# Kernel optimization log

Measured on AMD Instinct MI355X. Metric: run time of the kernel, lower is better.

## Reference

```python
import jax, jax.numpy as jnp
import numpy as np

B, T, C = 4, 4096, 1024
H, G = 16, 8
HS = C // H      # head size = 64
GT = T // G      # group_t = 512
KAPX = 1         # k_apx


def causal_attn(q, k, v):
    # q,k,v: [..., L, d]; causal softmax attention within last two dims
    d = q.shape[-1]
    s = jnp.einsum('...qd,...kd->...qk', q, k) / jnp.sqrt(jnp.asarray(d, q.dtype))
    mask = jnp.tril(jnp.ones((s.shape[-2], s.shape[-1]), dtype=bool))
    s = jnp.where(mask, s, jnp.asarray(-1e30, s.dtype))
    return jnp.einsum('...qk,...kd->...qd', jax.nn.softmax(s, axis=-1), v)


def apply_rope(x, cos, sin):
    # x: [B,H,T,HS]; cos/sin: [T,HS//2]; interleaved (even,odd) complex pairs
    xr = x.reshape(x.shape[:-1] + (HS // 2, 2))
    r, i = xr[..., 0], xr[..., 1]
    c = cos[None, None]
    s = sin[None, None]
    return jnp.stack([r * c - i * s, r * s + i * c], axis=-1).reshape(x.shape)


def setup_inputs() -> dict:
    key = jax.random.key(0)
    k1, k2, k3, k4, k5, k6 = jax.random.split(key, 6)
    x = jax.random.normal(k1, (B, T, C), jnp.float32)
    lim = 1.0 / np.sqrt(C)
    Wqkv = jax.random.uniform(k2, (C, 3 * C), jnp.float32, -lim, lim)
    Wo = jax.random.uniform(k3, (C, C), jnp.float32, -lim, lim)
    # init_() uses std = 1/sqrt(last_dim) = 1/sqrt(k_apx) = 1
    q_proj = jax.random.uniform(k4, (GT, KAPX), jnp.float32, -1.0, 1.0)
    k_proj = jax.random.uniform(k5, (GT, KAPX), jnp.float32, -1.0, 1.0)
    v_proj = jax.random.uniform(k6, (GT, KAPX), jnp.float32, -1.0, 1.0)
    inv = 1.0 / (10000.0 ** (np.arange(0, HS, 2) / HS))
    ang = np.outer(np.arange(T), inv)
    freqs_cos = jnp.asarray(np.cos(ang), jnp.float32)
    freqs_sin = jnp.asarray(np.sin(ang), jnp.float32)
    return dict(x=x, Wqkv=Wqkv, Wo=Wo, q_proj=q_proj, k_proj=k_proj,
                v_proj=v_proj, freqs_cos=freqs_cos, freqs_sin=freqs_sin)


def reference(x, Wqkv, Wo, q_proj, k_proj, v_proj, freqs_cos, freqs_sin):
    q, k, v = jnp.split(x @ Wqkv, 3, axis=-1)          # each [B,T,C]
    q = q.reshape(B, T, H, HS).transpose(0, 2, 1, 3)    # [B,H,T,HS]
    k = k.reshape(B, T, H, HS).transpose(0, 2, 1, 3)
    q = apply_rope(q, freqs_cos, freqs_sin)
    k = apply_rope(k, freqs_cos, freqs_sin)
    # torch .view on contiguous [B,H,T,HS]: raw row-major reinterpretation
    q = q.reshape(B, G, GT, H, HS).transpose(0, 3, 1, 2, 4)  # [B,H,G,GT,HS]
    k = k.reshape(B, G, GT, H, HS).transpose(0, 3, 1, 2, 4)
    v = v.reshape(B, G, GT, H, HS).transpose(0, 3, 1, 2, 4)  # v viewed from [B,T,C]
    # its_time branch: learned time-pooling of all but last group
    qb = jnp.einsum('bhgtc,tk->bhgkc', q[:, :, :-1], q_proj)  # [B,H,G-1,1,HS]
    kb = jnp.einsum('bhgtc,tk->bhgkc', k[:, :, :-1], k_proj)
    vb = jnp.einsum('bhgtc,tk->bhgkc', v[:, :, :-1], v_proj)
    o = causal_attn(q, k, v)          # block-local causal attention [B,H,G,GT,HS]
    vb = causal_attn(qb, kb, vb)      # compressed block attention [B,H,G-1,1,HS]
    o = o.reshape(B, H, G * GT, HS).transpose(0, 2, 1, 3).reshape(B, T, C)
    out = o @ Wo                       # dropout=0 (eval)
    return (out, qb, kb, vb)
```

## Files before the change

### kernel.cpp

```cpp
#include <hip/hip_runtime.h>


typedef float  float4_t  __attribute__((ext_vector_type(4)));
typedef short  bfrag     __attribute__((ext_vector_type(8)));
typedef unsigned short ushort8 __attribute__((ext_vector_type(8)));

#define MFMA_BF16(A, B, C) __builtin_amdgcn_mfma_f32_16x16x32_bf16((A), (B), (C), 0, 0, 0)

__device__ __forceinline__ unsigned short f2bf(float f) {
  union { float f; unsigned u; } v; v.f = f;
  return (unsigned short)((v.u + 0x7FFFu + ((v.u >> 16) & 1u)) >> 16);
}
__device__ __forceinline__ float bf2f(unsigned short h) {
  union { unsigned u; float f; } v; v.u = ((unsigned)h) << 16; return v.f;
}
__device__ __forceinline__ void async16(const void* g, void* l) {
  __builtin_amdgcn_global_load_lds(
      (const __attribute__((address_space(1))) unsigned int*)(unsigned long long)g,
      (__attribute__((address_space(3))) unsigned int*)(unsigned long long)l,
      16, 0, 0);
}

__global__ __launch_bounds__(256) void cvt_kernel(const float* __restrict__ in,
                                                  unsigned short* __restrict__ out, int n8) {
  int i = blockIdx.x * 256 + threadIdx.x;
  if (i >= n8) return;
  const float4_t* p = (const float4_t*)in + (size_t)i * 2;
  float4_t a = p[0], c = p[1];
  ushort8 r;
  r[0] = f2bf(a[0]); r[1] = f2bf(a[1]); r[2] = f2bf(a[2]); r[3] = f2bf(a[3]);
  r[4] = f2bf(c[0]); r[5] = f2bf(c[1]); r[6] = f2bf(c[2]); r[7] = f2bf(c[3]);
  *((ushort8*)out + i) = r;
}

__global__ void transpose_cvt_kernel(const float* __restrict__ in,
                                     unsigned short* __restrict__ out, int R, int C) {
  __shared__ float t[32][33];
  int bc = blockIdx.x * 32, br = blockIdx.y * 32;
  int x = threadIdx.x, y = threadIdx.y;
  for (int i = 0; i < 32; i += 8) t[y + i][x] = in[(size_t)(br + y + i) * C + bc + x];
  __syncthreads();
  for (int i = 0; i < 32; i += 8) out[(size_t)(bc + y + i) * R + br + x] = f2bf(t[x][y + i]);
}

__global__ void transpose2_f32_kernel(const float* __restrict__ a,
                                      const float* __restrict__ b,
                                      float* __restrict__ oa, float* __restrict__ ob_,
                                      int R, int C) {
  const float* in = blockIdx.z ? b : a;
  float* out = blockIdx.z ? ob_ : oa;
  __shared__ float t[32][33];
  int bc = blockIdx.x * 32, br = blockIdx.y * 32;
  int x = threadIdx.x, y = threadIdx.y;
  for (int i = 0; i < 32; i += 8) t[y + i][x] = in[(size_t)(br + y + i) * C + bc + x];
  __syncthreads();
  for (int i = 0; i < 32; i += 8) out[(size_t)(bc + y + i) * R + br + x] = t[x][y + i];
}

__device__ __forceinline__ void gemm_core(const unsigned short* __restrict__ A,
                                          const unsigned short* __restrict__ BT,
                                          int bm0, int bn0, int K,
                                          unsigned short* As, unsigned short* Bs,
                                          float4_t acc[4][4]) {
  int tid = threadIdx.x, w = tid >> 6;
  int lane = tid & 63, quad = lane >> 4, l16 = lane & 15;
  int wm = w >> 1, wn = w & 1;
  int rr = tid >> 2, xx = tid & 3;
  for (int k0 = 0; k0 < K; k0 += 32) {
    __syncthreads();
    {
      int r0 = rr,       s0 = xx ^ ((r0 >> 1) & 3);
      int r1 = rr + 64,  s1 = xx ^ ((r1 >> 1) & 3);
      async16(&A [(size_t)(bm0 + r0) * K + k0 + s0 * 8], &As[(size_t)(w * 64) * 8]);
      async16(&A [(size_t)(bm0 + r1) * K + k0 + s1 * 8], &As[(size_t)(256 + w * 64) * 8]);
      async16(&BT[(size_t)(bn0 + r0) * K + k0 + s0 * 8], &Bs[(size_t)(w * 64) * 8]);
      async16(&BT[(size_t)(bn0 + r1) * K + k0 + s1 * 8], &Bs[(size_t)(256 + w * 64) * 8]);
    }
    __syncthreads();
    bfrag af[4], bf_[4];
    for (int i = 0; i < 4; ++i) {
      int rm = wm * 64 + i * 16 + l16;
      af[i]  = *(const bfrag*)&As[(size_t)(rm * 4 + (quad ^ ((rm >> 1) & 3))) * 8];
      int rn = wn * 64 + i * 16 + l16;
      bf_[i] = *(const bfrag*)&Bs[(size_t)(rn * 4 + (quad ^ ((rn >> 1) & 3))) * 8];
    }
    for (int i = 0; i < 4; ++i)
      for (int j = 0; j < 4; ++j)
        acc[i][j] = MFMA_BF16(af[i], bf_[j], acc[i][j]);
  }
}

__global__ __launch_bounds__(256) void gemm1_kernel(const unsigned short* __restrict__ xb,
    const unsigned short* __restrict__ wqkvT,
    const float* __restrict__ fcT, const float* __restrict__ fsT,
    unsigned short* __restrict__ q5, unsigned short* __restrict__ k5,
    unsigned short* __restrict__ v5) {
  __shared__ __align__(16) unsigned short As[128 * 32];
  __shared__ __align__(16) unsigned short Bs[128 * 32];
  __shared__ __align__(16) float Es[4 * 1088];
  float4_t acc[4][4];
  for (int i = 0; i < 4; ++i) for (int j = 0; j < 4; ++j)
    acc[i][j] = (float4_t){0.f, 0.f, 0.f, 0.f};
  int bn0 = blockIdx.x * 128, bm0 = blockIdx.y * 128;
  gemm_core(xb, wqkvT, bm0, bn0, 1024, As, Bs, acc);

  int tid = threadIdx.x, w = tid >> 6, lane = tid & 63, quad = lane >> 4, l16 = lane & 15;
  int wm = w >> 1, wn = w & 1;

  for (int i = 0; i < 4; ++i) {
    int t0 = (bm0 + wm * 64 + i * 16 + quad * 4) & 4095;
    for (int j = 0; j < 4; ++j) {
      int gcol = bn0 + wn * 64 + j * 16 + l16;
      if (gcol < 2048) {
        int ci = (gcol & 63) >> 1;
        const float4_t c4 = *(const float4_t*)&fcT[(size_t)ci * 4096 + t0];
        const float4_t s4 = *(const float4_t*)&fsT[(size_t)ci * 4096 + t0];
        for (int r = 0; r < 4; ++r) {
          float val = acc[i][j][r];
          float partner = __shfl_xor(val, 1);
          float c = c4[r], s = s4[r];
          acc[i][j][r] = (gcol & 1) ? fmaf(partner, s, val * c)
                                    : fmaf(-partner, s, val * c);
        }
      }
    }
  }

  float* slice = &Es[w * 1088];
  for (int i = 0; i < 4; ++i) {
    for (int j = 0; j < 4; ++j)
      for (int r = 0; r < 4; ++r)
        slice[(quad * 4 + r) * 68 + j * 16 + l16] = acc[i][j][r];
    for (int m = 0; m < 2; ++m) {
      int rl = m * 8 + (lane >> 3);
      int cb = (lane & 7) * 8;
      const float* rp = &slice[rl * 68 + cb];
      ushort8 outv;
      outv[0] = f2bf(rp[0]); outv[1] = f2bf(rp[1]);
      outv[2] = f2bf(rp[2]); outv[3] = f2bf(rp[3]);
      outv[4] = f2bf(rp[4]); outv[5] = f2bf(rp[5]);
      outv[6] = f2bf(rp[6]); outv[7] = f2bf(rp[7]);
      int grow = bm0 + wm * 64 + i * 16 + rl;
      int b = grow >> 12, t = grow & 4095;
      int gcol = bn0 + wn * 64 + cb;
      if (gcol < 2048) {
        int cc = gcol & 1023;
        int ho = cc >> 6, hs0 = cc & 63;
        size_t idx = ((((size_t)b * 16 + (t & 15)) * 8 + (ho >> 1)) * 512 +
                      (((ho & 1) << 8) | (t >> 4))) * 64 + hs0;
        if (gcol < 1024) *(ushort8*)&q5[idx] = outv;
        else             *(ushort8*)&k5[idx] = outv;
      } else {
        int cc = gcol - 2048;
        size_t idx = ((((size_t)b * 16 + (cc >> 6)) * 8 + (t >> 9)) * 512 +
                      (t & 511)) * 64 + (cc & 63);
        *(ushort8*)&v5[idx] = outv;
      }
    }
  }
}

__global__ __launch_bounds__(256) void gemm2_kernel(const unsigned short* __restrict__ ob,
    const unsigned short* __restrict__ woT, float* __restrict__ outp) {
  __shared__ __align__(16) unsigned short As[128 * 32];
  __shared__ __align__(16) unsigned short Bs[128 * 32];
  float4_t acc[4][4];
  for (int i = 0; i < 4; ++i) for (int j = 0; j < 4; ++j)
    acc[i][j] = (float4_t){0.f, 0.f, 0.f, 0.f};
  int bn0 = blockIdx.x * 128, bm0 = blockIdx.y * 128;
  gemm_core(ob, woT, bm0, bn0, 1024, As, Bs, acc);
  int tid = threadIdx.x, w = tid >> 6, lane = tid & 63, quad = lane >> 4, l16 = lane & 15;
  int wm = w >> 1, wn = w & 1;
  for (int i = 0; i < 4; ++i)
    for (int j = 0; j < 4; ++j)
      for (int r = 0; r < 4; ++r)
        outp[(size_t)(bm0 + wm * 64 + i * 16 + quad * 4 + r) * 1024 +
             bn0 + wn * 64 + j * 16 + l16] = acc[i][j][r];
}

__global__ __launch_bounds__(256) void attn_kernel(const unsigned short* __restrict__ q5,
    const unsigned short* __restrict__ k5, const unsigned short* __restrict__ v5,
    unsigned short* __restrict__ ob) {
  __shared__ __align__(16) unsigned short Ks[128 * 64];
  __shared__ __align__(16) unsigned short VTs[64 * 136];
  __shared__ __align__(16) unsigned short Ps[4 * 16 * 136];
  int bx = blockIdx.x;
  int qt = bx & 7, g = (bx >> 3) & 7, h = (bx >> 6) & 15, b = bx >> 10;
  int tid = threadIdx.x, w = tid >> 6, lane = tid & 63, quad = lane >> 4, l16 = lane & 15;
  size_t base = ((((size_t)b * 16 + h) * 8 + g) * 512) * 64;
  const unsigned short* Q = q5 + base;
  const unsigned short* K = k5 + base;
  const unsigned short* V = v5 + base;

  int qrow = qt * 64 + w * 16 + l16;
  bfrag qf0 = *(const bfrag*)&Q[(size_t)qrow * 64 + quad * 8];
  bfrag qf1 = *(const bfrag*)&Q[(size_t)qrow * 64 + 32 + quad * 8];

  float4_t acc[4];
#pragma unroll
  for (int i = 0; i < 4; ++i) acc[i] = (float4_t){0.f, 0.f, 0.f, 0.f};
  float m_i[4] = {-1e30f, -1e30f, -1e30f, -1e30f};
  float l_i[4] = {0.f, 0.f, 0.f, 0.f};

  int skey = tid >> 3, sx = tid & 7, ss = sx ^ (skey & 7);
  int kp = tid & 63, hsg = tid >> 6;
  unsigned short* Pw = &Ps[w * 2176];
  int ntiles = (qt + 2) >> 1;

  for (int kt = 0; kt < ntiles; ++kt) {
    __syncthreads();
#pragma unroll
    for (int c = 0; c < 4; ++c)
      async16(&K[(size_t)(kt * 128 + 32 * c + skey) * 64 + ss * 8],
              &Ks[(size_t)(c * 256 + w * 64) * 8]);
    {
      const unsigned short* vp0 = &V[(size_t)(kt * 128 + kp * 2) * 64 + hsg * 16];
      ushort8 va0 = *(const ushort8*)vp0;
      ushort8 va1 = *(const ushort8*)(vp0 + 8);
      ushort8 vb0 = *(const ushort8*)(vp0 + 64);
      ushort8 vb1 = *(const ushort8*)(vp0 + 72);
#pragma unroll
      for (int e = 0; e < 8; ++e) {
        *(unsigned*)&VTs[(size_t)(hsg * 16 + e) * 136 + kp * 2] =
            (unsigned)va0[e] | ((unsigned)vb0[e] << 16);
        *(unsigned*)&VTs[(size_t)(hsg * 16 + 8 + e) * 136 + kp * 2] =
            (unsigned)va1[e] | ((unsigned)vb1[e] << 16);
      }
    }
    __syncthreads();

    float4_t s[8];
#pragma unroll
    for (int c = 0; c < 8; ++c) s[c] = (float4_t){0.f, 0.f, 0.f, 0.f};
    {
      int sl0 = l16 * 8 + (quad ^ (l16 & 7));
      int sl1 = l16 * 8 + ((4 + quad) ^ (l16 & 7));
#pragma unroll
      for (int c = 0; c < 8; ++c) {
        s[c] = MFMA_BF16(qf0, *(const bfrag*)&Ks[(size_t)(sl0 + 128 * c) * 8], s[c]);
        s[c] = MFMA_BF16(qf1, *(const bfrag*)&Ks[(size_t)(sl1 + 128 * c) * 8], s[c]);
      }
    }

    int qa = qt * 64 + w * 16 + quad * 4;
    int kb0 = kt * 128 + l16;
#pragma unroll
    for (int r = 0; r < 4; ++r) {
      float vv[8];
#pragma unroll
      for (int c = 0; c < 8; ++c) {
        vv[c] = s[c][r] * 0.125f;
        if (kb0 + 16 * c > qa + r) vv[c] = -1e30f;
      }
      float tm = fmaxf(fmaxf(fmaxf(vv[0], vv[1]), fmaxf(vv[2], vv[3])),
                       fmaxf(fmaxf(vv[4], vv[5]), fmaxf(vv[6], vv[7])));
      tm = fmaxf(tm, __shfl_xor(tm, 1));
      tm = fmaxf(tm, __shfl_xor(tm, 2));
      tm = fmaxf(tm, __shfl_xor(tm, 4));
      tm = fmaxf(tm, __shfl_xor(tm, 8));
      float nm = fmaxf(m_i[r], tm);
      float alpha = __expf(m_i[r] - nm);
      m_i[r] = nm;
      float p[8], rs = 0.f;
#pragma unroll
      for (int c = 0; c < 8; ++c) { p[c] = __expf(vv[c] - nm); rs += p[c]; }
      rs += __shfl_xor(rs, 1);
      rs += __shfl_xor(rs, 2);
      rs += __shfl_xor(rs, 4);
      rs += __shfl_xor(rs, 8);
      l_i[r] = l_i[r] * alpha + rs;
      acc[0][r] *= alpha; acc[1][r] *= alpha; acc[2][r] *= alpha; acc[3][r] *= alpha;
      int pr = (quad * 4 + r) * 136 + l16;
#pragma unroll
      for (int c = 0; c < 8; ++c) Pw[pr + 16 * c] = f2bf(p[c]);
    }
    bfrag pf[4];
#pragma unroll
    for (int c = 0; c < 4; ++c)
      pf[c] = *(const bfrag*)&Pw[(size_t)l16 * 136 + 32 * c + quad * 8];
#pragma unroll
    for (int ht = 0; ht < 4; ++ht) {
#pragma unroll
      for (int c = 0; c < 4; ++c) {
        bfrag vf = *(const bfrag*)&VTs[(size_t)(ht * 16 + l16) * 136 + 32 * c + quad * 8];
        acc[ht] = MFMA_BF16(pf[c], vf, acc[ht]);
      }
    }
  }

  int orow = b * 4096 + g * 512 + qt * 64 + w * 16 + quad * 4;
#pragma unroll
  for (int ht = 0; ht < 4; ++ht)
#pragma unroll
    for (int r = 0; r < 4; ++r)
      ob[(size_t)(orow + r) * 1024 + h * 64 + ht * 16 + l16] = f2bf(acc[ht][r] / l_i[r]);
}

__global__ __launch_bounds__(1024) void pools_kernel(const unsigned short* __restrict__ q5,
    const unsigned short* __restrict__ k5, const unsigned short* __restrict__ v5,
    const float* __restrict__ qp, const float* __restrict__ kp,
    const float* __restrict__ vp, float* __restrict__ outp) {
  __shared__ float red[3][16][64];
  int g = blockIdx.x, h = blockIdx.y, b = blockIdx.z;
  int hs = threadIdx.x & 63, tc = threadIdx.x >> 6;
  size_t base = ((((size_t)b * 16 + h) * 8 + g) * 512) * 64 + hs;
  float aq = 0.f, ak = 0.f, av = 0.f;
  int t0 = tc * 32;
  for (int t = t0; t < t0 + 32; ++t) {
    size_t o = base + (size_t)t * 64;
    aq = fmaf(bf2f(q5[o]), qp[t], aq);
    ak = fmaf(bf2f(k5[o]), kp[t], ak);
    av = fmaf(bf2f(v5[o]), vp[t], av);
  }
  red[0][tc][hs] = aq;
  red[1][tc][hs] = ak;
  red[2][tc][hs] = av;
  __syncthreads();
  if (tc < 3) {
    float a = 0.f;
    for (int c = 0; c < 16; ++c) a += red[tc][c][hs];
    size_t oi = (((size_t)b * 16 + h) * 7 + g) * 64 + hs;
    size_t off = (tc == 0) ? 0 : (tc == 1) ? 28672 : 57344;
    outp[16777216 + off + oi] = a;
  }
}

extern "C" void kernel_launch(void* const* d_in, const int* in_sizes, int n_in,
                              void* d_out, int out_size, void* d_ws, size_t ws_size,
                              hipStream_t stream) {
  (void)in_sizes; (void)n_in; (void)out_size; (void)ws_size;
  const float* x    = (const float*)d_in[0];
  const float* Wqkv = (const float*)d_in[1];
  const float* Wo   = (const float*)d_in[2];
  const float* qp   = (const float*)d_in[3];
  const float* kp   = (const float*)d_in[4];
  const float* vp   = (const float*)d_in[5];
  const float* fc   = (const float*)d_in[6];
  const float* fs   = (const float*)d_in[7];
  float* outp = (float*)d_out;

  char* ws = (char*)d_ws;
  unsigned short* xb    = (unsigned short*)(ws);
  unsigned short* wqkvT = (unsigned short*)(ws + 33554432);
  unsigned short* woT   = (unsigned short*)(ws + 39845888);
  unsigned short* q5    = (unsigned short*)(ws + 41943040);
  unsigned short* k5    = (unsigned short*)(ws + 75497472);
  unsigned short* v5    = (unsigned short*)(ws + 109051904);
  unsigned short* ob    = xb;

  float* fcT = outp;
  float* fsT = outp + 131072;

  cvt_kernel<<<8192, 256, 0, stream>>>(x, xb, 2097152);
  transpose_cvt_kernel<<<dim3(96, 32), dim3(32, 8), 0, stream>>>(Wqkv, wqkvT, 1024, 3072);
  transpose_cvt_kernel<<<dim3(32, 32), dim3(32, 8), 0, stream>>>(Wo, woT, 1024, 1024);
  transpose2_f32_kernel<<<dim3(1, 128, 2), dim3(32, 8), 0, stream>>>(fc, fs, fcT, fsT, 4096, 32);
  gemm1_kernel<<<dim3(24, 128), 256, 0, stream>>>(xb, wqkvT, fcT, fsT, q5, k5, v5);
  attn_kernel<<<4096, 256, 0, stream>>>(q5, k5, v5, ob);
  pools_kernel<<<dim3(7, 16, 4), 1024, 0, stream>>>(q5, k5, v5, qp, kp, vp, outp);
  gemm2_kernel<<<dim3(8, 128), 256, 0, stream>>>(ob, woT, outp);
}
```

Before: 502.4 us.

## Store QKV in natural row-major layout and gather scattered rows in attention

The QKV GEMM epilogue now writes one contiguous [B*T, 3072] bf16 buffer instead of scattering into three head/group-permuted arrays. The attention and pooling kernels index this buffer directly, reproducing the torch view reinterpretation through strided row addressing. This makes the epilogue stores simple and contiguous. In exchange, attention K/Q loads become strided gathers, each row 16 rows apart with a 3072-element pitch, which may hurt coalescing and cache locality.

```diff
diff --git a/kernel.cpp b/kernel.cpp
--- a/kernel.cpp
+++ b/kernel.cpp
@@ -93,8 +93,7 @@
 __global__ __launch_bounds__(256) void gemm1_kernel(const unsigned short* __restrict__ xb,
     const unsigned short* __restrict__ wqkvT,
     const float* __restrict__ fcT, const float* __restrict__ fsT,
-    unsigned short* __restrict__ q5, unsigned short* __restrict__ k5,
-    unsigned short* __restrict__ v5) {
+    unsigned short* __restrict__ qkv) {
   __shared__ __align__(16) unsigned short As[128 * 32];
   __shared__ __align__(16) unsigned short Bs[128 * 32];
   __shared__ __align__(16) float Es[4 * 1088];
@@ -141,21 +140,8 @@
       outv[4] = f2bf(rp[4]); outv[5] = f2bf(rp[5]);
       outv[6] = f2bf(rp[6]); outv[7] = f2bf(rp[7]);
       int grow = bm0 + wm * 64 + i * 16 + rl;
-      int b = grow >> 12, t = grow & 4095;
       int gcol = bn0 + wn * 64 + cb;
-      if (gcol < 2048) {
-        int cc = gcol & 1023;
-        int ho = cc >> 6, hs0 = cc & 63;
-        size_t idx = ((((size_t)b * 16 + (t & 15)) * 8 + (ho >> 1)) * 512 +
-                      (((ho & 1) << 8) | (t >> 4))) * 64 + hs0;
-        if (gcol < 1024) *(ushort8*)&q5[idx] = outv;
-        else             *(ushort8*)&k5[idx] = outv;
-      } else {
-        int cc = gcol - 2048;
-        size_t idx = ((((size_t)b * 16 + (cc >> 6)) * 8 + (t >> 9)) * 512 +
-                      (t & 511)) * 64 + (cc & 63);
-        *(ushort8*)&v5[idx] = outv;
-      }
+      *(ushort8*)&qkv[(size_t)grow * 3072 + gcol] = outv;
     }
   }
 }
@@ -178,8 +164,7 @@
              bn0 + wn * 64 + j * 16 + l16] = acc[i][j][r];
 }
 
-__global__ __launch_bounds__(256) void attn_kernel(const unsigned short* __restrict__ q5,
-    const unsigned short* __restrict__ k5, const unsigned short* __restrict__ v5,
+__global__ __launch_bounds__(256) void attn_kernel(const unsigned short* __restrict__ qkv,
     unsigned short* __restrict__ ob) {
   __shared__ __align__(16) unsigned short Ks[128 * 64];
   __shared__ __align__(16) unsigned short VTs[64 * 136];
@@ -187,14 +172,14 @@
   int bx = blockIdx.x;
   int qt = bx & 7, g = (bx >> 3) & 7, h = (bx >> 6) & 15, b = bx >> 10;
   int tid = threadIdx.x, w = tid >> 6, lane = tid & 63, quad = lane >> 4, l16 = lane & 15;
-  size_t base = ((((size_t)b * 16 + h) * 8 + g) * 512) * 64;
-  const unsigned short* Q = q5 + base;
-  const unsigned short* K = k5 + base;
-  const unsigned short* V = v5 + base;
+
+  const unsigned short* QKb = qkv + ((size_t)b * 4096 + h) * 3072 + g * 128;
+  const unsigned short* Vb  = qkv + ((size_t)(b * 4096 + g * 512)) * 3072 + 2048 + h * 64;
 
   int qrow = qt * 64 + w * 16 + l16;
-  bfrag qf0 = *(const bfrag*)&Q[(size_t)qrow * 64 + quad * 8];
-  bfrag qf1 = *(const bfrag*)&Q[(size_t)qrow * 64 + 32 + quad * 8];
+  const unsigned short* Qr = QKb + ((size_t)((qrow & 255) << 4)) * 3072 + (qrow >> 8) * 64;
+  bfrag qf0 = *(const bfrag*)&Qr[quad * 8];
+  bfrag qf1 = *(const bfrag*)&Qr[32 + quad * 8];
 
   float4_t acc[4];
 #pragma unroll
@@ -210,15 +195,17 @@
   for (int kt = 0; kt < ntiles; ++kt) {
     __syncthreads();
 #pragma unroll
-    for (int c = 0; c < 4; ++c)
-      async16(&K[(size_t)(kt * 128 + 32 * c + skey) * 64 + ss * 8],
+    for (int c = 0; c < 4; ++c) {
+      int krow = kt * 128 + 32 * c + skey;
+      async16(&QKb[((size_t)((krow & 255) << 4)) * 3072 + (krow >> 8) * 64 + 1024 + ss * 8],
               &Ks[(size_t)(c * 256 + w * 64) * 8]);
+    }
     {
-      const unsigned short* vp0 = &V[(size_t)(kt * 128 + kp * 2) * 64 + hsg * 16];
+      const unsigned short* vp0 = Vb + (size_t)(kt * 128 + kp * 2) * 3072 + hsg * 16;
       ushort8 va0 = *(const ushort8*)vp0;
       ushort8 va1 = *(const ushort8*)(vp0 + 8);
-      ushort8 vb0 = *(const ushort8*)(vp0 + 64);
-      ushort8 vb1 = *(const ushort8*)(vp0 + 72);
+      ushort8 vb0 = *(const ushort8*)(vp0 + 3072);
+      ushort8 vb1 = *(const ushort8*)(vp0 + 3080);
 #pragma unroll
       for (int e = 0; e < 8; ++e) {
         *(unsigned*)&VTs[(size_t)(hsg * 16 + e) * 136 + kp * 2] =
@@ -296,21 +283,21 @@
       ob[(size_t)(orow + r) * 1024 + h * 64 + ht * 16 + l16] = f2bf(acc[ht][r] / l_i[r]);
 }
 
-__global__ __launch_bounds__(1024) void pools_kernel(const unsigned short* __restrict__ q5,
-    const unsigned short* __restrict__ k5, const unsigned short* __restrict__ v5,
+__global__ __launch_bounds__(1024) void pools_kernel(const unsigned short* __restrict__ qkv,
     const float* __restrict__ qp, const float* __restrict__ kp,
     const float* __restrict__ vp, float* __restrict__ outp) {
   __shared__ float red[3][16][64];
   int g = blockIdx.x, h = blockIdx.y, b = blockIdx.z;
   int hs = threadIdx.x & 63, tc = threadIdx.x >> 6;
-  size_t base = ((((size_t)b * 16 + h) * 8 + g) * 512) * 64 + hs;
+  const unsigned short* qb_ = qkv + ((size_t)b * 4096 + h) * 3072 + g * 128 + hs;
+  const unsigned short* vb_ = qkv + ((size_t)(b * 4096 + g * 512)) * 3072 + 2048 + h * 64 + hs;
   float aq = 0.f, ak = 0.f, av = 0.f;
   int t0 = tc * 32;
   for (int t = t0; t < t0 + 32; ++t) {
-    size_t o = base + (size_t)t * 64;
-    aq = fmaf(bf2f(q5[o]), qp[t], aq);
-    ak = fmaf(bf2f(k5[o]), kp[t], ak);
-    av = fmaf(bf2f(v5[o]), vp[t], av);
+    size_t qoff = ((size_t)((t & 255) << 4)) * 3072 + (t >> 8) * 64;
+    aq = fmaf(bf2f(qb_[qoff]), qp[t], aq);
+    ak = fmaf(bf2f(qb_[qoff + 1024]), kp[t], ak);
+    av = fmaf(bf2f(vb_[(size_t)t * 3072]), vp[t], av);
   }
   red[0][tc][hs] = aq;
   red[1][tc][hs] = ak;
@@ -343,9 +330,7 @@
   unsigned short* xb    = (unsigned short*)(ws);
   unsigned short* wqkvT = (unsigned short*)(ws + 33554432);
   unsigned short* woT   = (unsigned short*)(ws + 39845888);
-  unsigned short* q5    = (unsigned short*)(ws + 41943040);
-  unsigned short* k5    = (unsigned short*)(ws + 75497472);
-  unsigned short* v5    = (unsigned short*)(ws + 109051904);
+  unsigned short* qkv   = (unsigned short*)(ws + 41943040);
   unsigned short* ob    = xb;
 
   float* fcT = outp;
@@ -355,8 +340,8 @@
   transpose_cvt_kernel<<<dim3(96, 32), dim3(32, 8), 0, stream>>>(Wqkv, wqkvT, 1024, 3072);
   transpose_cvt_kernel<<<dim3(32, 32), dim3(32, 8), 0, stream>>>(Wo, woT, 1024, 1024);
   transpose2_f32_kernel<<<dim3(1, 128, 2), dim3(32, 8), 0, stream>>>(fc, fs, fcT, fsT, 4096, 32);
-  gemm1_kernel<<<dim3(24, 128), 256, 0, stream>>>(xb, wqkvT, fcT, fsT, q5, k5, v5);
-  attn_kernel<<<4096, 256, 0, stream>>>(q5, k5, v5, ob);
-  pools_kernel<<<dim3(7, 16, 4), 1024, 0, stream>>>(q5, k5, v5, qp, kp, vp, outp);
+  gemm1_kernel<<<dim3(24, 128), 256, 0, stream>>>(xb, wqkvT, fcT, fsT, qkv);
+  attn_kernel<<<4096, 256, 0, stream>>>(qkv, ob);
+  pools_kernel<<<dim3(7, 16, 4), 1024, 0, stream>>>(qkv, qp, kp, vp, outp);
   gemm2_kernel<<<dim3(8, 128), 256, 0, stream>>>(ob, woT, outp);
 }
```

Result: no change. 510.1 us (+1.5%).
